# Kernel tuning notes

Hardware: AMD Instinct MI355X
Metric: run time of the kernel (lower is better)

The kernel has to match this reference:

```python
import jax, jax.numpy as jnp
import numpy as np

B, S, HID = 8, 4096, 1024
NH, HD = 16, 64  # heads, head_dim
LN_EPS = 1e-12


def setup_inputs() -> dict:
    key = jax.random.key(0)
    ks = jax.random.split(key, 12)
    sd = 1.0 / np.sqrt(HID)
    return {
        "input_tensor": jax.random.normal(ks[0], (B, S, HID), jnp.float32),
        "attention_mask": jnp.ones((B, S), jnp.int32),
        "ln_gamma": jnp.ones((HID,), jnp.float32),
        "ln_beta": jnp.zeros((HID,), jnp.float32),
        "Wq": jax.random.normal(ks[1], (HID, HID), jnp.float32) * sd,
        "bq": jnp.zeros((HID,), jnp.float32),
        "Wk": jax.random.normal(ks[2], (HID, HID), jnp.float32) * sd,
        "bk": jnp.zeros((HID,), jnp.float32),
        "Wv": jax.random.normal(ks[3], (HID, HID), jnp.float32) * sd,
        "bv": jnp.zeros((HID,), jnp.float32),
        "Wo": jax.random.normal(ks[4], (HID, HID), jnp.float32) * sd,
        "bo": jnp.zeros((HID,), jnp.float32),
    }


def _layernorm(x, g, b):
    mu = jnp.mean(x, axis=-1, keepdims=True)
    var = jnp.mean(jnp.square(x - mu), axis=-1, keepdims=True)
    return (x - mu) * jax.lax.rsqrt(var + LN_EPS) * g + b


def reference(input_tensor, attention_mask, ln_gamma, ln_beta,
              Wq, bq, Wk, bk, Wv, bv, Wo, bo):
    # NOTE: attention_mask is accepted but unused, matching the original module.
    x = input_tensor
    x_norm = _layernorm(x, ln_gamma, ln_beta)
    # projections: query from normalized input, key/value from raw input
    q = (x_norm @ Wq.T + bq).reshape(B, S, NH, HD).transpose(0, 2, 1, 3)  # bhsd
    k = (x @ Wk.T + bk).reshape(B, S, NH, HD).transpose(0, 2, 1, 3)      # bhsd
    v = (x @ Wv.T + bv).reshape(B, S, NH, HD).transpose(0, 2, 1, 3)      # bhsd

    eq = jax.nn.elu(q)
    ek = jax.nn.elu(k)
    # per-token L2 norms over head_dim (matches norm over d in both layouts)
    eq = eq / jnp.linalg.norm(eq, axis=-1, keepdims=True)
    ek = ek / jnp.linalg.norm(ek, axis=-1, keepdims=True)

    # linear attention: Q (K^T V), never materializing [S,S]
    kv = jnp.einsum('bhsd,bhse->bhde', ek, v)          # [B,H,d,d]
    ctx = jnp.einsum('bhsd,bhde->bhse', eq, kv) / np.sqrt(HD)

    ctx = ctx.transpose(0, 2, 1, 3).reshape(B, S, HID)
    out = ctx @ Wo.T + bo
    return out + x  # residual (dropouts are identity in eval mode)
```

## Files before the change

kernel.cpp:

```cpp
#include <hip/hip_runtime.h>

typedef unsigned short u16;
typedef unsigned int   u32;
typedef __attribute__((ext_vector_type(8))) __bf16 bf16x8;
typedef __attribute__((ext_vector_type(4))) float  f32x4;

#define BQ   8
#define SQ   4096
#define NHQ  16
#define HIDD 1024
#define TOKN 32768

__device__ __forceinline__ u16 f2bf(float f){
  u32 u = __builtin_bit_cast(u32, f);
  u += 0x7fffu + ((u >> 16) & 1u);
  return (u16)(u >> 16);
}
__device__ __forceinline__ float bf2f(u16 h){
  return __builtin_bit_cast(float, (u32)h << 16);
}
__device__ __forceinline__ void gl16(const void* g, void* l){
  __builtin_amdgcn_global_load_lds((const __attribute__((address_space(1))) void*)g,
                                   (__attribute__((address_space(3))) void*)l, 16, 0, 0);
}
#define MFMA(a,b,c) __builtin_amdgcn_mfma_f32_16x16x32_bf16((a),(b),(c),0,0,0)

__global__ __launch_bounds__(256) void k_prep(const float* __restrict__ wk,
    const float* __restrict__ wv, const float* __restrict__ wo,
    const float* __restrict__ Wq, const float* __restrict__ gam,
    const float* __restrict__ bet, const float* __restrict__ bq,
    u16* __restrict__ okv, u16* __restrict__ oo,
    u16* __restrict__ wqb, float* __restrict__ cq, float* __restrict__ dq){
  const int t = threadIdx.x;
  if (blockIdx.x < 3072){
    const int sel = blockIdx.x >> 10;
    const int i = ((blockIdx.x & 1023) << 8) + t;
    const float* in = (sel == 0) ? wk : (sel == 1) ? wv : wo;
    u16* o = (sel == 0) ? okv : (sel == 1) ? (okv + 1024 * 1024) : oo;
    float4 v = ((const float4*)in)[i];
    ushort4 r;
    r.x = f2bf(v.x); r.y = f2bf(v.y); r.z = f2bf(v.z); r.w = f2bf(v.w);
    ((ushort4*)o)[i] = r;
  } else {
    const int j = blockIdx.x - 3072;
    const float4 wvq = ((const float4*)(Wq + (size_t)j * 1024))[t];
    const float4 gv = ((const float4*)gam)[t];
    const float4 bv = ((const float4*)bet)[t];
    ushort4 r;
    r.x = f2bf(wvq.x * gv.x); r.y = f2bf(wvq.y * gv.y);
    r.z = f2bf(wvq.z * gv.z); r.w = f2bf(wvq.w * gv.w);
    ((ushort4*)(wqb + (size_t)j * 1024))[t] = r;
    float sc = bf2f(r.x) + bf2f(r.y) + bf2f(r.z) + bf2f(r.w);
    float sd = wvq.x * bv.x + wvq.y * bv.y + wvq.z * bv.z + wvq.w * bv.w;
    #pragma unroll
    for (int o = 1; o < 64; o <<= 1){ sc += __shfl_xor(sc, o); sd += __shfl_xor(sd, o); }
    __shared__ float sm[8];
    const int lane = t & 63, wid = t >> 6;
    if (lane == 0){ sm[wid] = sc; sm[wid + 4] = sd; }
    __syncthreads();
    if (t == 0){
      cq[j] = sm[0] + sm[1] + sm[2] + sm[3];
      dq[j] = sm[4] + sm[5] + sm[6] + sm[7] + bq[j];
    }
  }
}

__global__ __launch_bounds__(256) void k_ln(const float* __restrict__ x,
    u16* __restrict__ xbf, float* __restrict__ mur, float* __restrict__ rsd){
  const int row = blockIdx.x, t = threadIdx.x;
  const float4 v = ((const float4*)(x + (size_t)row * HIDD))[t];
  float s  = v.x + v.y + v.z + v.w;
  float ss = v.x*v.x + v.y*v.y + v.z*v.z + v.w*v.w;
  #pragma unroll
  for (int o = 1; o < 64; o <<= 1){ s += __shfl_xor(s, o); ss += __shfl_xor(ss, o); }
  __shared__ float sm[8];
  const int lane = t & 63, wid = t >> 6;
  if (lane == 0){ sm[wid] = s; sm[wid + 4] = ss; }
  __syncthreads();
  s  = sm[0] + sm[1] + sm[2] + sm[3];
  ss = sm[4] + sm[5] + sm[6] + sm[7];
  const float mu   = s * (1.f / 1024.f);
  const float var  = ss * (1.f / 1024.f) - mu * mu;
  const float rstd = rsqrtf(var + 1e-12f);
  if (t == 0){ mur[row] = mu * rstd; rsd[row] = rstd; }
  ushort4 xo;
  xo.x = f2bf(v.x); xo.y = f2bf(v.y); xo.z = f2bf(v.z); xo.w = f2bf(v.w);
  ((ushort4*)(xbf + (size_t)row * HIDD))[t] = xo;
}

struct GP {
  const u16* A; const u16* W; const float* b1; const float* b2;
  int nsplit, lgNB, LDC, nblk; u16* outb; u16* voutT;
  const float* cq; const float* dq; const float* mur; const float* rsd;
};

template<int RES, int SPLIT>
__global__ __launch_bounds__(512, 2) void k_gemm256(GP p0, GP p1, int seg0,
    const u16* __restrict__ residb, float* __restrict__ outf){
  __shared__ union {
    u16 st[2][2][16384];
    float cep[8][1056];
    float cep2[8][2112];
  } sm;

  const GP& p = (blockIdx.x < seg0) ? p0 : p1;
  const int bseg = (blockIdx.x < seg0) ? blockIdx.x : blockIdx.x - seg0;
  const u16* __restrict__ A = p.A;
  const u16* __restrict__ W = p.W;
  const int lgNB = p.lgNB, LDC = p.LDC;

  const int wg = ((bseg & 7) * (p.nblk >> 3)) + (bseg >> 3);
  const int m0 = (wg >> lgNB) << 8;
  const int n0 = (wg & ((1 << lgNB) - 1)) << 8;

  const int t = threadIdx.x, lane = t & 63, wid = t >> 6;
  const int ln15 = lane & 15, hi = lane >> 4;
  const int wr = wid >> 2, wc = wid & 3;
  const int lg = lane & 7, lr = lane >> 3;

  auto stage = [&](int buf, int op, const u16* __restrict__ src, int rowoff, int kt){
    #pragma unroll
    for (int i = 0; i < 4; i++){
      const int cb  = ((i << 3) + wid) << 6;
      const int row = (cb >> 3) + lr;
      const int g   = lg ^ lr;
      gl16(src + (size_t)(rowoff + row) * HIDD + (kt << 6) + (g << 3),
           &sm.st[buf][op][cb << 3]);
    }
  };
  auto stageH = [&](int buf, int op, const u16* __restrict__ src, int rowoff, int kt, int half){
    #pragma unroll
    for (int i2 = 0; i2 < 2; i2++){
      const int i = (half << 1) + i2;
      const int cb  = ((i << 3) + wid) << 6;
      const int row = (cb >> 3) + lr;
      const int g   = lg ^ lr;
      gl16(src + (size_t)(rowoff + row) * HIDD + (kt << 6) + (g << 3),
           &sm.st[buf][op][cb << 3]);
    }
  };
  #define RD_A(c,m,ks) (*(const bf16x8*)&sm.st[c][0][(((wr << 7) + ((m) << 4) + ln15) << 6) + \
      (((((ks) << 2) + hi) ^ (lane & 7)) << 3)])
  #define RD_B(c,n,ks) (*(const bf16x8*)&sm.st[c][1][(((wc << 6) + ((n) << 4) + ln15) << 6) + \
      (((((ks) << 2) + hi) ^ (lane & 7)) << 3)])
  #define BARF do { asm volatile("" ::: "memory"); __builtin_amdgcn_s_barrier(); asm volatile("" ::: "memory"); } while(0)

  f32x4 acc[8][4] = {};

  stage(0, 0, A, m0, 0);
  stage(0, 1, W, n0, 0);
  stage(1, 1, W, n0, 1);
  asm volatile("s_waitcnt vmcnt(4)" ::: "memory");
  BARF;

  const int NT = HIDD / 64;
  if constexpr (SPLIT == 0){
    for (int kt = 0; kt < NT; ++kt){
      const int c = kt & 1;
      bf16x8 af[4][2], bq[4][2];
      #pragma unroll
      for (int m = 0; m < 4; m++){ af[m][0] = RD_A(c, m, 0); af[m][1] = RD_A(c, m, 1); }
      #pragma unroll
      for (int n = 0; n < 4; n++){ bq[n][0] = RD_B(c, n, 0); bq[n][1] = RD_B(c, n, 1); }
      const int ka = kt + 1 < NT ? kt + 1 : NT - 1;
      stage(c ^ 1, 0, A, m0, ka);
      __builtin_amdgcn_s_setprio(1);
      #pragma unroll
      for (int m = 0; m < 4; m++)
        #pragma unroll
        for (int n = 0; n < 4; n++){
          acc[m][n] = MFMA(af[m][0], bq[n][0], acc[m][n]);
          acc[m][n] = MFMA(af[m][1], bq[n][1], acc[m][n]);
        }
      __builtin_amdgcn_s_setprio(0);
      BARF;
      #pragma unroll
      for (int m = 0; m < 4; m++){ af[m][0] = RD_A(c, m + 4, 0); af[m][1] = RD_A(c, m + 4, 1); }
      const int kb = kt + 2 < NT ? kt + 2 : NT - 1;
      stage(c, 1, W, n0, kb);
      __builtin_amdgcn_s_setprio(1);
      #pragma unroll
      for (int m = 0; m < 4; m++)
        #pragma unroll
        for (int n = 0; n < 4; n++){
          acc[m + 4][n] = MFMA(af[m][0], bq[n][0], acc[m + 4][n]);
          acc[m + 4][n] = MFMA(af[m][1], bq[n][1], acc[m + 4][n]);
        }
      __builtin_amdgcn_s_setprio(0);
      asm volatile("s_waitcnt vmcnt(4)" ::: "memory");
      BARF;
    }
  } else {
    for (int kt = 0; kt < NT; ++kt){
      const int c = kt & 1;
      const int ka  = kt + 1 < NT ? kt + 1 : NT - 1;
      const int kb2 = kt + 2 < NT ? kt + 2 : NT - 1;
      bf16x8 af[2][2], bq[4][2];
      af[0][0] = RD_A(c, 0, 0); af[0][1] = RD_A(c, 0, 1);
      af[1][0] = RD_A(c, 1, 0); af[1][1] = RD_A(c, 1, 1);
      #pragma unroll
      for (int n = 0; n < 4; n++){ bq[n][0] = RD_B(c, n, 0); bq[n][1] = RD_B(c, n, 1); }
      stageH(c ^ 1, 0, A, m0, ka, 0);
      __builtin_amdgcn_s_setprio(1);
      #pragma unroll
      for (int m = 0; m < 2; m++)
        #pragma unroll
        for (int n = 0; n < 4; n++){
          acc[m][n] = MFMA(af[m][0], bq[n][0], acc[m][n]);
          acc[m][n] = MFMA(af[m][1], bq[n][1], acc[m][n]);
        }
      __builtin_amdgcn_s_setprio(0);
      BARF;
      af[0][0] = RD_A(c, 2, 0); af[0][1] = RD_A(c, 2, 1);
      af[1][0] = RD_A(c, 3, 0); af[1][1] = RD_A(c, 3, 1);
      stageH(c ^ 1, 0, A, m0, ka, 1);
      __builtin_amdgcn_s_setprio(1);
      #pragma unroll
      for (int m = 0; m < 2; m++)
        #pragma unroll
        for (int n = 0; n < 4; n++){
          acc[m + 2][n] = MFMA(af[m][0], bq[n][0], acc[m + 2][n]);
          acc[m + 2][n] = MFMA(af[m][1], bq[n][1], acc[m + 2][n]);
        }
      __builtin_amdgcn_s_setprio(0);
      BARF;
      af[0][0] = RD_A(c, 4, 0); af[0][1] = RD_A(c, 4, 1);
      af[1][0] = RD_A(c, 5, 0); af[1][1] = RD_A(c, 5, 1);
      stageH(c, 1, W, n0, kb2, 0);
      __builtin_amdgcn_s_setprio(1);
      #pragma unroll
      for (int m = 0; m < 2; m++)
        #pragma unroll
        for (int n = 0; n < 4; n++){
          acc[m + 4][n] = MFMA(af[m][0], bq[n][0], acc[m + 4][n]);
          acc[m + 4][n] = MFMA(af[m][1], bq[n][1], acc[m + 4][n]);
        }
      __builtin_amdgcn_s_setprio(0);
      BARF;
      af[0][0] = RD_A(c, 6, 0); af[0][1] = RD_A(c, 6, 1);
      af[1][0] = RD_A(c, 7, 0); af[1][1] = RD_A(c, 7, 1);
      stageH(c, 1, W, n0, kb2, 1);
      __builtin_amdgcn_s_setprio(1);
      #pragma unroll
      for (int m = 0; m < 2; m++)
        #pragma unroll
        for (int n = 0; n < 4; n++){
          acc[m + 6][n] = MFMA(af[m][0], bq[n][0], acc[m + 6][n]);
          acc[m + 6][n] = MFMA(af[m][1], bq[n][1], acc[m + 6][n]);
        }
      __builtin_amdgcn_s_setprio(0);
      asm volatile("s_waitcnt vmcnt(4)" ::: "memory");
      BARF;
    }
  }
  #undef RD_A
  #undef RD_B

  asm volatile("s_waitcnt vmcnt(0)" ::: "memory");
  BARF;

  const float* bp = (n0 < p.nsplit) ? p.b1 : (p.b2 - p.nsplit);
  float bn[4];
  #pragma unroll
  for (int n = 0; n < 4; n++) bn[n] = bp[n0 + (wc << 6) + (n << 4) + ln15];

  if constexpr (RES){
    float* cw = &sm.cep[wid][0];
    const int rr = lane >> 3, cb8 = (lane & 7) << 3;
    #pragma unroll
    for (int m = 0; m < 8; m++){
      #pragma unroll
      for (int n = 0; n < 4; n++)
        #pragma unroll
        for (int r = 0; r < 4; r++)
          cw[((hi << 2) + r) * 66 + (n << 4) + ln15] = acc[m][n][r] + bn[n];
      #pragma unroll
      for (int j = 0; j < 2; j++){
        const int row = (j << 3) + rr;
        const size_t gr = (size_t)(m0 + (wr << 7) + (m << 4) + row);
        const size_t gidx = gr * LDC + n0 + (wc << 6) + cb8;
        const size_t ridx = gr * HIDD + n0 + (wc << 6) + cb8;
        const uint4 rv = *(const uint4*)&residb[ridx];
        const u32 rr4[4] = {rv.x, rv.y, rv.z, rv.w};
        float4 o0, o1;
        o0.x = cw[row * 66 + cb8 + 0] + bf2f((u16)(rr4[0] & 0xffff));
        o0.y = cw[row * 66 + cb8 + 1] + bf2f((u16)(rr4[0] >> 16));
        o0.z = cw[row * 66 + cb8 + 2] + bf2f((u16)(rr4[1] & 0xffff));
        o0.w = cw[row * 66 + cb8 + 3] + bf2f((u16)(rr4[1] >> 16));
        o1.x = cw[row * 66 + cb8 + 4] + bf2f((u16)(rr4[2] & 0xffff));
        o1.y = cw[row * 66 + cb8 + 5] + bf2f((u16)(rr4[2] >> 16));
        o1.z = cw[row * 66 + cb8 + 6] + bf2f((u16)(rr4[3] & 0xffff));
        o1.w = cw[row * 66 + cb8 + 7] + bf2f((u16)(rr4[3] >> 16));
        *(float4*)&outf[gidx]     = o0;
        *(float4*)&outf[gidx + 4] = o1;
      }
    }
  } else if (p.voutT != nullptr && n0 >= p.nsplit){
    float* cw = &sm.cep2[wid][0];
    const int e0 = n0 - p.nsplit + (wc << 6);
    const int hh = e0 >> 6;
    u16* vt = p.voutT;
    #pragma unroll
    for (int mp = 0; mp < 4; mp++){
      #pragma unroll
      for (int mh = 0; mh < 2; mh++){
        const int m = (mp << 1) + mh;
        #pragma unroll
        for (int n = 0; n < 4; n++)
          #pragma unroll
          for (int r = 0; r < 4; r++)
            cw[((mh << 4) + (hi << 2) + r) * 66 + (n << 4) + ln15] = acc[m][n][r] + bn[n];
      }
      const int rg0 = m0 + (wr << 7) + (mp << 5);
      const int bb = rg0 >> 12, s0 = rg0 & 4095;
      u16* dst = vt + (((size_t)(bb << 4) + hh) * 64 + lane) * SQ + s0;
      #pragma unroll
      for (int j = 0; j < 4; j++){
        u32 ro[4];
        #pragma unroll
        for (int q = 0; q < 4; q++){
          float v0 = cw[((j << 3) + 2 * q    ) * 66 + lane];
          float v1 = cw[((j << 3) + 2 * q + 1) * 66 + lane];
          ro[q] = (u32)f2bf(v0) | ((u32)f2bf(v1) << 16);
        }
        uint4 o; o.x = ro[0]; o.y = ro[1]; o.z = ro[2]; o.w = ro[3];
        *(uint4*)&dst[j << 3] = o;
      }
    }
  } else {
    float* cw = &sm.cep[wid][0];
    const int rr = lane >> 3, cb8 = (lane & 7) << 3;
    u16* outb = p.outb;
    if (p.cq != nullptr){
      float cqn[4], dqn[4];
      #pragma unroll
      for (int n = 0; n < 4; n++){
        const int col = n0 + (wc << 6) + (n << 4) + ln15;
        cqn[n] = p.cq[col]; dqn[n] = p.dq[col];
      }
      #pragma unroll
      for (int m = 0; m < 8; m++){
        #pragma unroll
        for (int r = 0; r < 4; r++){
          const int grow = m0 + (wr << 7) + (m << 4) + (hi << 2) + r;
          const float mu = p.mur[grow], rs = p.rsd[grow];
          #pragma unroll
          for (int n = 0; n < 4; n++)
            cw[((hi << 2) + r) * 66 + (n << 4) + ln15] = rs * acc[m][n][r] - mu * cqn[n] + dqn[n];
        }
        #pragma unroll
        for (int j = 0; j < 2; j++){
          const int row = (j << 3) + rr;
          u32 ro[4];
          #pragma unroll
          for (int pq = 0; pq < 4; pq++){
            float v0 = cw[row * 66 + cb8 + 2 * pq];
            float v1 = cw[row * 66 + cb8 + 2 * pq + 1];
            ro[pq] = (u32)f2bf(v0) | ((u32)f2bf(v1) << 16);
          }
          uint4 o; o.x = ro[0]; o.y = ro[1]; o.z = ro[2]; o.w = ro[3];
          *(uint4*)&outb[(size_t)(m0 + (wr << 7) + (m << 4) + row) * LDC
                         + n0 + (wc << 6) + cb8] = o;
        }
      }
    } else {
      #pragma unroll
      for (int m = 0; m < 8; m++){
        #pragma unroll
        for (int n = 0; n < 4; n++)
          #pragma unroll
          for (int r = 0; r < 4; r++)
            cw[((hi << 2) + r) * 66 + (n << 4) + ln15] = acc[m][n][r] + bn[n];
        #pragma unroll
        for (int j = 0; j < 2; j++){
          const int row = (j << 3) + rr;
          u32 ro[4];
          #pragma unroll
          for (int pq = 0; pq < 4; pq++){
            float v0 = cw[row * 66 + cb8 + 2 * pq];
            float v1 = cw[row * 66 + cb8 + 2 * pq + 1];
            ro[pq] = (u32)f2bf(v0) | ((u32)f2bf(v1) << 16);
          }
          uint4 o; o.x = ro[0]; o.y = ro[1]; o.z = ro[2]; o.w = ro[3];
          *(uint4*)&outb[(size_t)(m0 + (wr << 7) + (m << 4) + row) * LDC
                         + n0 + (wc << 6) + cb8] = o;
        }
      }
    }
  }
  #undef BARF
}

__global__ __launch_bounds__(256) void k_transposeK(const u16* __restrict__ kb,
                                                    u16* __restrict__ ekT){
  __shared__ float tile[64][65];
  __shared__ float pr[64][4];
  __shared__ float rn[64];
  const int sb = blockIdx.x << 6, h = blockIdx.y, b = blockIdx.z;
  const int t = threadIdx.x;
  {
    const int tok = t >> 2, q = t & 3;
    const u16* src = kb + (size_t)(b * SQ + sb + tok) * 1024 + (h << 6) + (q << 4);
    uint4 u0 = *(const uint4*)src;
    uint4 u1 = *(const uint4*)(src + 8);
    u32 uu[8] = {u0.x, u0.y, u0.z, u0.w, u1.x, u1.y, u1.z, u1.w};
    float ss = 0.f;
    #pragma unroll
    for (int i = 0; i < 8; i++){
      float f0 = bf2f((u16)(uu[i] & 0xffff));
      float f1 = bf2f((u16)(uu[i] >> 16));
      f0 = f0 > 0.f ? f0 : expm1f(f0);
      f1 = f1 > 0.f ? f1 : expm1f(f1);
      ss += f0 * f0 + f1 * f1;
      tile[tok][(q << 4) + 2*i]     = f0;
      tile[tok][(q << 4) + 2*i + 1] = f1;
    }
    pr[tok][q] = ss;
  }
  __syncthreads();
  if (t < 64) rn[t] = rsqrtf(pr[t][0] + pr[t][1] + pr[t][2] + pr[t][3]);
  __syncthreads();
  const int d = t >> 2, sq2 = (t & 3) << 4;
  u16* dst = ekT + ((size_t)(b * NHQ + h) * 64 + d) * SQ + sb + sq2;
  u32 ro[8];
  #pragma unroll
  for (int i = 0; i < 8; i++){
    float v0 = tile[sq2 + 2*i][d]     * rn[sq2 + 2*i];
    float v1 = tile[sq2 + 2*i + 1][d] * rn[sq2 + 2*i + 1];
    ro[i] = (u32)f2bf(v0) | ((u32)f2bf(v1) << 16);
  }
  uint4 o0; o0.x = ro[0]; o0.y = ro[1]; o0.z = ro[2]; o0.w = ro[3];
  uint4 o1; o1.x = ro[4]; o1.y = ro[5]; o1.z = ro[6]; o1.w = ro[7];
  *(uint4*)dst = o0;
  *(uint4*)(dst + 8) = o1;
}

__global__ __launch_bounds__(256) void k_kv(const u16* __restrict__ vT, const u16* __restrict__ ekT,
                                            float* __restrict__ kvP){
  const int half = blockIdx.x & 1, bh = blockIdx.x >> 1;
  const u16* Av = vT  + (size_t)bh * 64 * SQ;
  const u16* Bk = ekT + (size_t)bh * 64 * SQ;
  const int lane = threadIdx.x & 63, wid = threadIdx.x >> 6;
  const int ln15 = lane & 15, hi = lane >> 4;
  f32x4 acc[4][4] = {};
  const int kb = (half << 11) + (wid << 9);
  for (int ks = 0; ks < 16; ++ks){
    const int k0 = kb + (ks << 5) + (hi << 3);
    bf16x8 af[4], bfr[4];
    #pragma unroll
    for (int m = 0; m < 4; m++) af[m]  = *(const bf16x8*)(Av + (size_t)((m << 4) + ln15) * SQ + k0);
    #pragma unroll
    for (int n = 0; n < 4; n++) bfr[n] = *(const bf16x8*)(Bk + (size_t)((n << 4) + ln15) * SQ + k0);
    #pragma unroll
    for (int m = 0; m < 4; m++)
      #pragma unroll
      for (int n = 0; n < 4; n++)
        acc[m][n] = MFMA(af[m], bfr[n], acc[m][n]);
  }
  __shared__ float red[64][64];
  for (int w = 0; w < 4; ++w){
    if (wid == w){
      #pragma unroll
      for (int m = 0; m < 4; m++)
        #pragma unroll
        for (int n = 0; n < 4; n++)
          #pragma unroll
          for (int r = 0; r < 4; r++){
            int row = (m << 4) + (hi << 2) + r;
            int col = (n << 4) + ln15;
            if (w == 0) red[row][col] = acc[m][n][r];
            else        red[row][col] += acc[m][n][r];
          }
    }
    __syncthreads();
  }
  float* dst = kvP + (size_t)blockIdx.x * 4096;
  const int tt = threadIdx.x;
  #pragma unroll
  for (int i = 0; i < 16; i++){
    int idx = tt * 16 + i;
    dst[idx] = red[idx >> 6][idx & 63];
  }
}

__global__ __launch_bounds__(256) void k_kvr(const float* __restrict__ kvP,
                                             u16* __restrict__ kvT){
  const int bh = blockIdx.x, t = threadIdx.x;
  const float* p0 = kvP + (size_t)(bh << 1) * 4096;
  const float* p1 = p0 + 4096;
  u16* dst = kvT + (size_t)bh * 4096;
  #pragma unroll
  for (int i = 0; i < 2; i++){
    const int idx = (i << 11) + (t << 3);
    const float4 a0 = *(const float4*)&p0[idx];
    const float4 a1 = *(const float4*)&p0[idx + 4];
    const float4 b0 = *(const float4*)&p1[idx];
    const float4 b1 = *(const float4*)&p1[idx + 4];
    u32 ro[4];
    ro[0] = (u32)f2bf((a0.x + b0.x) * 0.125f) | ((u32)f2bf((a0.y + b0.y) * 0.125f) << 16);
    ro[1] = (u32)f2bf((a0.z + b0.z) * 0.125f) | ((u32)f2bf((a0.w + b0.w) * 0.125f) << 16);
    ro[2] = (u32)f2bf((a1.x + b1.x) * 0.125f) | ((u32)f2bf((a1.y + b1.y) * 0.125f) << 16);
    ro[3] = (u32)f2bf((a1.z + b1.z) * 0.125f) | ((u32)f2bf((a1.w + b1.w) * 0.125f) << 16);
    uint4 o; o.x = ro[0]; o.y = ro[1]; o.z = ro[2]; o.w = ro[3];
    *(uint4*)&dst[idx] = o;
  }
}

__global__ __launch_bounds__(256) void k_ctx(const u16* __restrict__ q, const u16* __restrict__ kvT,
                                             u16* __restrict__ ctx){
  __shared__ u16 Alds[1024 * 8];
  __shared__ u16 Blds[512 * 8];
  __shared__ float prn[128][2];
  const int sb = blockIdx.x << 7;
  const int h = blockIdx.y, b = blockIdx.z;
  const int bh = (b << 4) + h;
  const int t = threadIdx.x, lane = t & 63, wid = t >> 6;
  const int ln15 = lane & 15, hi = lane >> 4;
  {
    uint4 va[4]; uint4 vb[2];
    #pragma unroll
    for (int i = 0; i < 4; i++){
      int c = (wid << 6) + (i << 8) + lane;
      int g = c >> 7, row = c & 127;
      va[i] = *(const uint4*)(q + (size_t)(b * SQ + sb + row) * HIDD + (h << 6) + g * 8);
    }
    #pragma unroll
    for (int i = 0; i < 2; i++){
      int c = (wid << 6) + (i << 8) + lane;
      int g = c >> 6, row = c & 63;
      vb[i] = *(const uint4*)(kvT + (size_t)bh * 4096 + (row << 6) + g * 8);
    }
    #pragma unroll
    for (int i = 0; i < 4; i++)
      *(uint4*)&Alds[((wid << 6) + (i << 8) + lane) * 8] = va[i];
    #pragma unroll
    for (int i = 0; i < 2; i++)
      *(uint4*)&Blds[((wid << 6) + (i << 8) + lane) * 8] = vb[i];
  }
  __syncthreads();
  {
    const int row = t & 127, half = t >> 7;
    float vals[4][8]; float ss = 0.f;
    #pragma unroll
    for (int g4 = 0; g4 < 4; g4++){
      const int g = (half << 2) + g4;
      uint4 u = *(const uint4*)&Alds[((g << 7) + row) * 8];
      u32 uu[4] = {u.x, u.y, u.z, u.w};
      #pragma unroll
      for (int i = 0; i < 4; i++){
        float f0 = bf2f((u16)(uu[i] & 0xffff));
        float f1 = bf2f((u16)(uu[i] >> 16));
        f0 = f0 > 0.f ? f0 : expm1f(f0);
        f1 = f1 > 0.f ? f1 : expm1f(f1);
        vals[g4][2*i] = f0; vals[g4][2*i+1] = f1;
        ss += f0 * f0 + f1 * f1;
      }
    }
    prn[row][half] = ss;
    __syncthreads();
    const float rn = rsqrtf(prn[row][0] + prn[row][1]);
    #pragma unroll
    for (int g4 = 0; g4 < 4; g4++){
      const int g = (half << 2) + g4;
      u32 ro[4];
      #pragma unroll
      for (int i = 0; i < 4; i++)
        ro[i] = (u32)f2bf(vals[g4][2*i] * rn) | ((u32)f2bf(vals[g4][2*i+1] * rn) << 16);
      uint4 o; o.x = ro[0]; o.y = ro[1]; o.z = ro[2]; o.w = ro[3];
      *(uint4*)&Alds[((g << 7) + row) * 8] = o;
    }
  }
  __syncthreads();
  f32x4 acc[2][4] = {};
  #pragma unroll
  for (int k2 = 0; k2 < 2; k2++){
    const int g = (k2 << 2) + hi;
    bf16x8 af[2], bfr[4];
    #pragma unroll
    for (int m = 0; m < 2; m++) af[m]  = *(const bf16x8*)&Alds[((g << 7) + (wid << 5) + (m << 4) + ln15) * 8];
    #pragma unroll
    for (int n = 0; n < 4; n++) bfr[n] = *(const bf16x8*)&Blds[((g << 6) + (n << 4) + ln15) * 8];
    #pragma unroll
    for (int m = 0; m < 2; m++)
      #pragma unroll
      for (int n = 0; n < 4; n++)
        acc[m][n] = MFMA(af[m], bfr[n], acc[m][n]);
  }
  #pragma unroll
  for (int m = 0; m < 2; m++)
    #pragma unroll
    for (int n = 0; n < 4; n++)
      #pragma unroll
      for (int r = 0; r < 4; r++){
        int srow = sb + (wid << 5) + (m << 4) + (hi << 2) + r;
        int col  = (n << 4) + ln15;
        ctx[(size_t)(b * SQ + srow) * HIDD + (h << 6) + col] = f2bf(acc[m][n][r]);
      }
}

extern "C" void kernel_launch(void* const* d_in, const int* in_sizes, int n_in,
                              void* d_out, int out_size, void* d_ws, size_t ws_size,
                              hipStream_t stream){
  const float* x   = (const float*)d_in[0];
  const float* lng = (const float*)d_in[2];
  const float* lnb = (const float*)d_in[3];
  const float* Wq  = (const float*)d_in[4];
  const float* bq  = (const float*)d_in[5];
  const float* Wk  = (const float*)d_in[6];
  const float* bk  = (const float*)d_in[7];
  const float* Wv  = (const float*)d_in[8];
  const float* bv  = (const float*)d_in[9];
  const float* Wo  = (const float*)d_in[10];
  const float* bo  = (const float*)d_in[11];
  float* out = (float*)d_out;

  char* w = (char*)d_ws;
  const size_t MB = 1ull << 20;
  u16* wqb  = (u16*)(w + 0   * MB);
  u16* wkvb = (u16*)(w + 2   * MB);
  u16* wob  = (u16*)(w + 6   * MB);
  u16* xbf  = (u16*)(w + 8   * MB);
  u16* xnbf = (u16*)(w + 72  * MB);
  u16* qb   = (u16*)(w + 136 * MB);
  u16* kb   = (u16*)(w + 200 * MB);
  u16* vT   = (u16*)(w + 264 * MB);
  u16* kvT  = (u16*)(w + 328 * MB);
  float* murstd = (float*)(w + 330 * MB);
  float* rstdv  = (float*)(w + 331 * MB);
  float* cqv    = (float*)(w + 332 * MB);
  float* dqv    = (float*)(w + 333 * MB);
  float* kvP    = (float*)(w + 336 * MB);
  u16* ekT = xnbf;
  u16* ctx = kb;

  k_prep<<<4096, 256, 0, stream>>>(Wk, Wv, Wo, Wq, lng, lnb, bq, wkvb, wob, wqb, cqv, dqv);
  k_ln<<<TOKN, 256, 0, stream>>>(x, xbf, murstd, rstdv);

  GP pq  = { xbf, wqb,  bq, bq, 1 << 30, 2, 1024, 512,  qb, nullptr, cqv, dqv, murstd, rstdv };
  GP pkv = { xbf, wkvb, bk, bv, 1024,    3, 1024, 1024, kb, vT,      nullptr, nullptr, nullptr, nullptr };
  k_gemm256<0, 0><<<1536, 512, 0, stream>>>(pq, pkv, 512, nullptr, nullptr);

  k_transposeK<<<dim3(64, 16, 8), 256, 0, stream>>>(kb, ekT);
  k_kv<<<256, 256, 0, stream>>>(vT, ekT, kvP);
  k_kvr<<<128, 256, 0, stream>>>(kvP, kvT);
  k_ctx<<<dim3(32, 16, 8), 256, 0, stream>>>(qb, kvT, ctx);

  GP po = { ctx, wob, bo, bo, 1 << 30, 2, 1024, 512, nullptr, nullptr,
            nullptr, nullptr, nullptr, nullptr };
  k_gemm256<1, 1><<<512, 512, 0, stream>>>(po, po, 512, xbf, out);

  (void)in_sizes; (void)n_in; (void)out_size; (void)ws_size;
}
```

Measured before the change: 658.8 us.

## Split KV reduction four ways and fold partial-sum reduction into ctx kernel

The K^T V kernel now splits the sequence into four partitions per batch-head instead of two, launching 512 blocks instead of 256 for more parallelism. The separate reduction kernel that summed the partials and converted them to bf16 is removed. Each ctx block now reads the four fp32 partials directly, sums them, scales and converts them while filling its shared-memory tile. This removes one launch and an intermediate buffer round-trip, but every ctx block (32 per batch-head) now redoes the reduction and reads 4x fp32 data instead of one bf16 tile.

```diff
diff --git a/kernel.cpp b/kernel.cpp
--- a/kernel.cpp
+++ b/kernel.cpp
@@ -437,14 +437,14 @@
 
 __global__ __launch_bounds__(256) void k_kv(const u16* __restrict__ vT, const u16* __restrict__ ekT,
                                             float* __restrict__ kvP){
-  const int half = blockIdx.x & 1, bh = blockIdx.x >> 1;
+  const int qtr = blockIdx.x & 3, bh = blockIdx.x >> 2;
   const u16* Av = vT  + (size_t)bh * 64 * SQ;
   const u16* Bk = ekT + (size_t)bh * 64 * SQ;
   const int lane = threadIdx.x & 63, wid = threadIdx.x >> 6;
   const int ln15 = lane & 15, hi = lane >> 4;
   f32x4 acc[4][4] = {};
-  const int kb = (half << 11) + (wid << 9);
-  for (int ks = 0; ks < 16; ++ks){
+  const int kb = (qtr << 10) + (wid << 8);
+  for (int ks = 0; ks < 8; ++ks){
     const int k0 = kb + (ks << 5) + (hi << 3);
     bf16x8 af[4], bfr[4];
     #pragma unroll
@@ -483,30 +483,7 @@
   }
 }
 
-__global__ __launch_bounds__(256) void k_kvr(const float* __restrict__ kvP,
-                                             u16* __restrict__ kvT){
-  const int bh = blockIdx.x, t = threadIdx.x;
-  const float* p0 = kvP + (size_t)(bh << 1) * 4096;
-  const float* p1 = p0 + 4096;
-  u16* dst = kvT + (size_t)bh * 4096;
-  #pragma unroll
-  for (int i = 0; i < 2; i++){
-    const int idx = (i << 11) + (t << 3);
-    const float4 a0 = *(const float4*)&p0[idx];
-    const float4 a1 = *(const float4*)&p0[idx + 4];
-    const float4 b0 = *(const float4*)&p1[idx];
-    const float4 b1 = *(const float4*)&p1[idx + 4];
-    u32 ro[4];
-    ro[0] = (u32)f2bf((a0.x + b0.x) * 0.125f) | ((u32)f2bf((a0.y + b0.y) * 0.125f) << 16);
-    ro[1] = (u32)f2bf((a0.z + b0.z) * 0.125f) | ((u32)f2bf((a0.w + b0.w) * 0.125f) << 16);
-    ro[2] = (u32)f2bf((a1.x + b1.x) * 0.125f) | ((u32)f2bf((a1.y + b1.y) * 0.125f) << 16);
-    ro[3] = (u32)f2bf((a1.z + b1.z) * 0.125f) | ((u32)f2bf((a1.w + b1.w) * 0.125f) << 16);
-    uint4 o; o.x = ro[0]; o.y = ro[1]; o.z = ro[2]; o.w = ro[3];
-    *(uint4*)&dst[idx] = o;
-  }
-}
-
-__global__ __launch_bounds__(256) void k_ctx(const u16* __restrict__ q, const u16* __restrict__ kvT,
+__global__ __launch_bounds__(256) void k_ctx(const u16* __restrict__ q, const float* __restrict__ kvP,
                                              u16* __restrict__ ctx){
   __shared__ u16 Alds[1024 * 8];
   __shared__ u16 Blds[512 * 8];
@@ -524,11 +501,26 @@
       int g = c >> 7, row = c & 127;
       va[i] = *(const uint4*)(q + (size_t)(b * SQ + sb + row) * HIDD + (h << 6) + g * 8);
     }
+    const float* pp = kvP + ((size_t)bh << 14);
     #pragma unroll
     for (int i = 0; i < 2; i++){
       int c = (wid << 6) + (i << 8) + lane;
       int g = c >> 6, row = c & 63;
-      vb[i] = *(const uint4*)(kvT + (size_t)bh * 4096 + (row << 6) + g * 8);
+      const int eidx = (row << 6) + (g << 3);
+      float s[8] = {0.f, 0.f, 0.f, 0.f, 0.f, 0.f, 0.f, 0.f};
+      #pragma unroll
+      for (int qq = 0; qq < 4; qq++){
+        const float4 a = *(const float4*)&pp[(qq << 12) + eidx];
+        const float4 bq2 = *(const float4*)&pp[(qq << 12) + eidx + 4];
+        s[0] += a.x; s[1] += a.y; s[2] += a.z; s[3] += a.w;
+        s[4] += bq2.x; s[5] += bq2.y; s[6] += bq2.z; s[7] += bq2.w;
+      }
+      u32 ro[4];
+      #pragma unroll
+      for (int j = 0; j < 4; j++)
+        ro[j] = (u32)f2bf(s[2*j] * 0.125f) | ((u32)f2bf(s[2*j+1] * 0.125f) << 16);
+      uint4 o; o.x = ro[0]; o.y = ro[1]; o.z = ro[2]; o.w = ro[3];
+      vb[i] = o;
     }
     #pragma unroll
     for (int i = 0; i < 4; i++)
@@ -624,7 +616,6 @@
   u16* qb   = (u16*)(w + 136 * MB);
   u16* kb   = (u16*)(w + 200 * MB);
   u16* vT   = (u16*)(w + 264 * MB);
-  u16* kvT  = (u16*)(w + 328 * MB);
   float* murstd = (float*)(w + 330 * MB);
   float* rstdv  = (float*)(w + 331 * MB);
   float* cqv    = (float*)(w + 332 * MB);
@@ -641,9 +632,8 @@
   k_gemm256<0, 0><<<1536, 512, 0, stream>>>(pq, pkv, 512, nullptr, nullptr);
 
   k_transposeK<<<dim3(64, 16, 8), 256, 0, stream>>>(kb, ekT);
-  k_kv<<<256, 256, 0, stream>>>(vT, ekT, kvP);
-  k_kvr<<<128, 256, 0, stream>>>(kvP, kvT);
-  k_ctx<<<dim3(32, 16, 8), 256, 0, stream>>>(qb, kvT, ctx);
+  k_kv<<<512, 256, 0, stream>>>(vT, ekT, kvP);
+  k_ctx<<<dim3(32, 16, 8), 256, 0, stream>>>(qb, kvP, ctx);
 
   GP po = { ctx, wob, bo, bo, 1 << 30, 2, 1024, 512, nullptr, nullptr,
             nullptr, nullptr, nullptr, nullptr };
```

Measured after the change: 683.2 us. 1.04x slower.
